# Optimization experiments

Measured on AMD Instinct MI355X. Metric: run time of the kernel, lower is better.

Reference implementation:

```python
import jax, jax.numpy as jnp
import numpy as np

N = 50000      # nodes
E = 600000     # edges (before self loops)
F_IN = 128     # num_features
HID = 64       # num_hidden (per-head out channels of conv1)
HEADS = 8
NCLS = 16      # num_classes
NC = 16        # n_components (k_ricci feature dim)
NCP = 16       # n_components_p (e_poinc feature dim)


def _glorot(key, shape):
    lim = float(np.sqrt(6.0 / (shape[0] + shape[1])))
    return jax.random.uniform(key, shape, jnp.float32, -lim, lim)


def setup_inputs() -> dict:
    key = jax.random.key(0)
    ks = jax.random.split(key, 16)
    H1 = HEADS * HID  # 512
    return {
        "x": jax.random.normal(ks[0], (N, F_IN), jnp.float32),
        "edge_index": jax.random.randint(ks[1], (2, E), 0, N, jnp.int32),
        "alpha": jnp.ones((), jnp.float32),  # alpha_hp scalar
        "k_ricci": jax.random.normal(ks[2], (E + N, NC), jnp.float32),
        "e_poinc": jax.random.normal(ks[3], (N, NCP), jnp.float32),
        # conv1 params
        "W_src1": _glorot(ks[4], (F_IN, H1)),
        "h1_w1": _glorot(ks[5], (NC, HID)),
        "h1_w2": _glorot(ks[6], (HID, HID)),
        "h1_b2": jnp.zeros((HID,), jnp.float32),
        "p1_w1": _glorot(ks[7], (NCP, H1)),
        "p1_w2": _glorot(ks[8], (H1, H1)),
        "p1_b2": jnp.zeros((H1,), jnp.float32),
        "bias1": jnp.zeros((H1,), jnp.float32),
        # conv2 params (heads=1, concat=False)
        "W_src2": _glorot(ks[9], (H1, NCLS)),
        "h2_w1": _glorot(ks[10], (NC, NCLS)),
        "h2_w2": _glorot(ks[11], (NCLS, NCLS)),
        "h2_b2": jnp.zeros((NCLS,), jnp.float32),
        "p2_w1": _glorot(ks[12], (NCP, NCLS)),
        "p2_w2": _glorot(ks[13], (NCLS, NCLS)),
        "p2_b2": jnp.zeros((NCLS,), jnp.float32),
        "bias2": jnp.zeros((NCLS,), jnp.float32),
    }


def _segment_softmax(logits, seg, n):
    # PyG-style softmax over variable-sized segments, per channel.
    m = jax.ops.segment_max(logits, seg, num_segments=n)
    e = jnp.exp(logits - m[seg])
    s = jax.ops.segment_sum(e, seg, num_segments=n)
    return e / (s[seg] + 1e-16)


def _gat_layer(x, src, dst, k_ricci, e_poinc, alpha_hp,
               W_src, hw1, hw2, hb2, pw1, pw2, pb2, bias, H, C, concat):
    n = x.shape[0]
    xh = (x @ W_src).reshape(n, H, C)                                   # [N,H,C]
    # hmpnn MLP on per-edge Ricci features, then segment-softmax over SOURCE node
    edge_w = jax.nn.leaky_relu(k_ricci @ hw1, 0.2) @ hw2 + hb2          # [E',C]
    a = _segment_softmax(edge_w, src, n)                                # [E',C]
    msg = a[:, None, :] * xh[src]                                       # [E',H,C]
    agg = jax.ops.segment_sum(msg, dst, num_segments=n)                 # [N,H,C]
    out = agg.reshape(n, H * C) if concat else agg.mean(axis=1)
    out = out + bias
    # ham MLP on per-node Poincare features (+ extra leaky_relu, slope 0.01)
    p = jax.nn.leaky_relu(jax.nn.leaky_relu(e_poinc @ pw1, 0.2) @ pw2 + pb2, 0.01)
    return out + alpha_hp * p


def reference(x, edge_index, alpha, k_ricci, e_poinc,
              W_src1, h1_w1, h1_w2, h1_b2, p1_w1, p1_w2, p1_b2, bias1,
              W_src2, h2_w1, h2_w2, h2_b2, p2_w1, p2_w2, p2_b2, bias2):
    n = x.shape[0]
    loops = jnp.arange(n, dtype=edge_index.dtype)
    src = jnp.concatenate([edge_index[0], loops])   # add_self_loops
    dst = jnp.concatenate([edge_index[1], loops])
    h = _gat_layer(x, src, dst, k_ricci, e_poinc, alpha,
                   W_src1, h1_w1, h1_w2, h1_b2, p1_w1, p1_w2, p1_b2, bias1,
                   HEADS, HID, True)
    h = jax.nn.relu(h)
    o = _gat_layer(h, src, dst, k_ricci, e_poinc, alpha,
                   W_src2, h2_w1, h2_w2, h2_b2, p2_w1, p2_w2, p2_b2, bias2,
                   1, NCLS, False)
    return jax.nn.log_softmax(o, axis=1)
```

## Files before the change

kernel.cpp:

```cpp
#include <hip/hip_runtime.h>
#include <math.h>

#define N_NODES 50000
#define M_PAD   50048
#define N_EDGES 600000
#define E_TOT   650000
#define F_IN    128
#define HID     64
#define HEADS   8
#define H1      512
#define NCLS    16
#define NC      16
#define NCP     16
#define NBLK    ((N_NODES + 255) / 256)
#define FRNG    (N_NODES / 8)
#define FBPR    128
#define FPER    ((E_TOT + FBPR - 1) / FBPR)

typedef unsigned short u16;
typedef unsigned char  u8;
typedef __attribute__((ext_vector_type(8))) short short8;
typedef __attribute__((ext_vector_type(4))) float f32x4;
typedef __attribute__((ext_vector_type(2))) float f32x2;

__device__ __forceinline__ float bf2f(u16 h) {
    return __uint_as_float(((unsigned)h) << 16);
}
__device__ __forceinline__ u16 f2bf(float f) {
    unsigned u = __float_as_uint(f);
    u += 0x7fffu + ((u >> 16) & 1u);
    return (u16)(u >> 16);
}
__device__ __forceinline__ int edge_src(const int* __restrict__ ei, int e) {
    return (e < N_EDGES) ? ei[e] : (e - N_EDGES);
}
__device__ __forceinline__ int edge_dst(const int* __restrict__ ei, int e) {
    return (e < N_EDGES) ? ei[N_EDGES + e] : (e - N_EDGES);
}

__device__ __forceinline__ void gload16(const void* g, void* l) {
    __builtin_amdgcn_global_load_lds(
        (const __attribute__((address_space(1))) unsigned int*)g,
        (__attribute__((address_space(3))) unsigned int*)l, 16, 0, 0);
}

__global__ __launch_bounds__(256) void count_k(const int* __restrict__ ei,
                                               int* __restrict__ src_cnt, int* __restrict__ dst_cnt) {
    int e = blockIdx.x * 256 + threadIdx.x;
    if (e >= E_TOT) return;
    atomicAdd(&src_cnt[edge_src(ei, e)], 1);
    atomicAdd(&dst_cnt[edge_dst(ei, e)], 1);
}

__global__ __launch_bounds__(256) void scanA_k(const int* __restrict__ src_cnt,
                                               const int* __restrict__ dst_cnt,
                                               int* __restrict__ partials) {
    int pass = blockIdx.x >= NBLK;
    int b = blockIdx.x - pass * NBLK;
    const int* cnt = pass ? dst_cnt : src_cnt;
    int idx = b * 256 + threadIdx.x;
    int v = (idx < N_NODES) ? cnt[idx] : 0;
    __shared__ int red[4];
    #pragma unroll
    for (int off = 32; off; off >>= 1) v += __shfl_down(v, off, 64);
    if ((threadIdx.x & 63) == 0) red[threadIdx.x >> 6] = v;
    __syncthreads();
    if (threadIdx.x == 0) partials[blockIdx.x] = red[0] + red[1] + red[2] + red[3];
}

__global__ __launch_bounds__(512) void scanB_k(int* __restrict__ partials) {
    __shared__ int lds[512];
    int t = threadIdx.x;
    int seg = t >> 8, i = t & 255;
    int v = (i < NBLK) ? partials[seg * NBLK + i] : 0;
    lds[t] = v;
    __syncthreads();
    for (int d = 1; d < 256; d <<= 1) {
        int x = (i >= d) ? lds[seg * 256 + i - d] : 0;
        __syncthreads();
        lds[t] += x;
        __syncthreads();
    }
    if (i < NBLK) partials[seg * NBLK + i] = lds[t] - v;
}

__global__ __launch_bounds__(256) void scanC_k(const int* __restrict__ src_cnt,
                                               const int* __restrict__ dst_cnt,
                                               const int* __restrict__ partials,
                                               int* __restrict__ src_off, int* __restrict__ dst_off) {
    int pass = blockIdx.x >= NBLK;
    int b = blockIdx.x - pass * NBLK;
    const int* cnt = pass ? dst_cnt : src_cnt;
    int* off = pass ? dst_off : src_off;
    int base = partials[blockIdx.x];
    __shared__ int lds[256];
    int t = threadIdx.x;
    int idx = b * 256 + t;
    int v = (idx < N_NODES) ? cnt[idx] : 0;
    lds[t] = v;
    __syncthreads();
    for (int d = 1; d < 256; d <<= 1) {
        int x = (t >= d) ? lds[t - d] : 0;
        __syncthreads();
        lds[t] += x;
        __syncthreads();
    }
    if (idx < N_NODES) off[idx] = base + lds[t] - v;
    if (b == 0 && t == 0) off[N_NODES] = E_TOT;
}

__global__ __launch_bounds__(256) void fillD_k(const int* __restrict__ ei,
                                               const int* __restrict__ dst_off, int* __restrict__ dst_cur,
                                               int* __restrict__ deid, int* __restrict__ dsrc) {
    const int range = blockIdx.x & 7, slice = blockIdx.x >> 3;
    const int d0 = range * FRNG, d1 = d0 + FRNG;
    const int e0 = slice * FPER;
    const int e1 = (e0 + FPER < E_TOT) ? e0 + FPER : E_TOT;
    for (int e = e0 + threadIdx.x; e < e1; e += 256) {
        int d = edge_dst(ei, e);
        if (d < d0 || d >= d1) continue;
        int rd = dst_off[d] + atomicAdd(&dst_cur[d], 1);
        deid[rd] = e;
        dsrc[rd] = edge_src(ei, e);
    }
}

__global__ __launch_bounds__(256) void fillS_k(const int* __restrict__ dsrc,
                                               const int* __restrict__ src_off, int* __restrict__ src_cur,
                                               int* __restrict__ src_list) {
    const int range = blockIdx.x & 7, slice = blockIdx.x >> 3;
    const int s0 = range * FRNG, s1 = s0 + FRNG;
    const int r0 = slice * FPER;
    const int r1 = (r0 + FPER < E_TOT) ? r0 + FPER : E_TOT;
    for (int rd = r0 + threadIdx.x; rd < r1; rd += 256) {
        int s = dsrc[rd];
        if (s < s0 || s >= s1) continue;
        src_list[src_off[s] + atomicAdd(&src_cur[s], 1)] = rd;
    }
}

__global__ __launch_bounds__(256) void conv_a_k(const float* __restrict__ A, u16* __restrict__ Ap,
                                                int M, int Mp, int K) {
    int i = blockIdx.x * 256 + threadIdx.x;
    int total = (K >> 3) * Mp;
    if (i >= total) return;
    int r = i % Mp;
    int kb = i / Mp;
    u16* o = Ap + (size_t)i * 8;
    u16 tmp[8];
    if (r < M) {
        const float* a = A + (size_t)r * K + kb * 8;
        #pragma unroll
        for (int j = 0; j < 8; ++j) tmp[j] = f2bf(a[j]);
    } else {
        #pragma unroll
        for (int j = 0; j < 8; ++j) tmp[j] = 0;
    }
    *(ushort4*)o = *(ushort4*)tmp;
    *(ushort4*)(o + 4) = *(ushort4*)(tmp + 4);
}

__global__ __launch_bounds__(256) void conv_b_k(const float* __restrict__ B, u16* __restrict__ Bp,
                                                int K, int N) {
    int i = blockIdx.x * 256 + threadIdx.x;
    int total = (K >> 3) * N;
    if (i >= total) return;
    int n = i % N;
    int kb = i / N;
    u16 tmp[8];
    #pragma unroll
    for (int j = 0; j < 8; ++j) tmp[j] = f2bf(B[(size_t)(kb * 8 + j) * N + n]);
    u16* o = Bp + (size_t)i * 8;
    *(ushort4*)o = *(ushort4*)tmp;
    *(ushort4*)(o + 4) = *(ushort4*)(tmp + 4);
}

__device__ __forceinline__ void wfrag_one(const float* W, u16* o, int i, int K, int N) {
    int j = i & 7, lane = (i >> 3) & 63, rest = i >> 9;
    int nt = rest % (N / 16), ks = rest / (N / 16);
    int lm = lane & 15, quad = lane >> 4;
    int k = ks * 32 + quad * 8 + j, n = nt * 16 + lm;
    o[i] = (k < K) ? f2bf(W[(size_t)k * N + n]) : (u16)0;
}
__global__ __launch_bounds__(256) void wfrag_all_k(
    const float* __restrict__ h1w1, const float* __restrict__ h1w2,
    const float* __restrict__ h2w1, const float* __restrict__ h2w2,
    u16* __restrict__ w1f, u16* __restrict__ w2f,
    u16* __restrict__ w3f, u16* __restrict__ w4f) {
    int i = blockIdx.x * 256 + threadIdx.x;
    if (i < 2048)      wfrag_one(h1w1, w1f, i, 16, 64);
    else if (i < 6144) wfrag_one(h1w2, w2f, i - 2048, 64, 64);
    else if (i < 6656) wfrag_one(h2w1, w3f, i - 6144, 16, 16);
    else if (i < 7168) wfrag_one(h2w2, w4f, i - 6656, 16, 16);
}

template<int EPI>
__global__ __launch_bounds__(256) void mfma_gemm_k(
    const u16* __restrict__ Ap, const u16* __restrict__ Bp, u16* __restrict__ C,
    int M, int Mp, int Nn, int K,
    const float* __restrict__ bias, const u16* __restrict__ extra,
    const float* __restrict__ bias2, const float* __restrict__ alpha_p)
{
    __shared__ __align__(16) u16 LB[4][4096];
    const int t = threadIdx.x;
    const int wave = t >> 6, lane = t & 63;
    const int wm = (wave >> 1) * 64, wn = (wave & 1) * 64;
    const int lm = lane & 15, quad = lane >> 4;

    const int nwg = (int)(gridDim.y << 2);
    const int bid = (int)(blockIdx.y * 4 + blockIdx.x);
    const int qq = nwg >> 3, rr8 = nwg & 7;
    const int xcd = bid & 7, idx = bid >> 3;
    const int wg = (xcd < rr8 ? xcd * (qq + 1) : rr8 * (qq + 1) + (xcd - rr8) * qq) + idx;
    const int bn = (wg & 3) * 128;
    const int bm = (wg >> 2) * 128;

    const char* Ab = (const char*)Ap;
    const char* Bb = (const char*)Bp;

    f32x4 acc[4][4] = {};
    const int NT = K >> 5;

    auto stage = [&](int buf, int ts) {
        const int kb0 = ts * 4;
        #pragma unroll
        for (int h = 0; h < 2; ++h) {
            const int ob = h * 4096 + wave * 1024;
            const int kb = kb0 + (ob >> 11);
            const int rem = (ob & 1024) + lane * 16;
            gload16(Ab + ((size_t)kb * Mp + bm) * 16 + rem, (char*)LB[buf] + ob);
            gload16(Bb + ((size_t)kb * Nn + bn) * 16 + rem, (char*)LB[2 + buf] + ob);
        }
    };
    auto compute = [&](int cb) {
        const u16* As = LB[cb];
        const u16* Bs = LB[2 + cb];
        short8 af[4], bfv[4];
        #pragma unroll
        for (int mi = 0; mi < 4; ++mi)
            af[mi] = *(const short8*)(As + quad * 1024 + (wm + mi * 16 + lm) * 8);
        #pragma unroll
        for (int nj = 0; nj < 4; ++nj)
            bfv[nj] = *(const short8*)(Bs + quad * 1024 + (wn + nj * 16 + lm) * 8);
        #pragma unroll
        for (int mi = 0; mi < 4; ++mi)
            #pragma unroll
            for (int nj = 0; nj < 4; ++nj)
                acc[mi][nj] = __builtin_amdgcn_mfma_f32_16x16x32_bf16(af[mi], bfv[nj], acc[mi][nj], 0, 0, 0);
    };

    stage(0, 0);
    __syncthreads();
    int cur = 0;
    for (int ts = 0; ts < NT - 1; ++ts) {
        stage(cur ^ 1, ts + 1);
        compute(cur);
        __syncthreads();
        cur ^= 1;
    }
    compute(cur);
    __syncthreads();

    float* Tf = (float*)LB;
    const int lrow = t & 63, chunk = t >> 6;
    const int col0 = chunk * 32;
    const float alpha = (EPI == 0) ? 0.f : *alpha_p;
    #pragma unroll
    for (int pass = 0; pass < 2; ++pass) {
        if ((wave >> 1) == pass) {
            #pragma unroll
            for (int mi = 0; mi < 4; ++mi)
                #pragma unroll
                for (int r4 = 0; r4 < 4; ++r4) {
                    const int lr = mi * 16 + quad * 4 + r4;
                    const int sw = (lr & 7) << 2;
                    #pragma unroll
                    for (int nj = 0; nj < 4; ++nj)
                        Tf[lr * 128 + ((wn + nj * 16 + lm) ^ sw)] = acc[mi][nj][r4];
                }
        }
        __syncthreads();
        const int rr = bm + pass * 64 + lrow;
        if (rr < M) {
            const int sw = (lrow & 7) << 2;
            float v[32];
            #pragma unroll
            for (int j4 = 0; j4 < 8; ++j4) {
                float4 f = *(const float4*)&Tf[lrow * 128 + ((col0 + j4 * 4) ^ sw)];
                v[j4 * 4] = f.x; v[j4 * 4 + 1] = f.y; v[j4 * 4 + 2] = f.z; v[j4 * 4 + 3] = f.w;
            }
            const int gc0 = bn + col0;
            u16 pk[32];
            if (EPI == 0) {
                #pragma unroll
                for (int j = 0; j < 32; ++j) pk[j] = f2bf(v[j]);
            } else {
                const u16* ex = extra + (size_t)rr * Nn + gc0;
                #pragma unroll
                for (int g = 0; g < 4; ++g) {
                    short8 e8 = *(const short8*)(ex + g * 8);
                    #pragma unroll
                    for (int j = 0; j < 8; ++j) {
                        const int cj = g * 8 + j;
                        float vv = v[cj] + bias[gc0 + cj];
                        vv = vv > 0.f ? vv : 0.01f * vv;
                        float o = bf2f((u16)e8[j]) + bias2[gc0 + cj] + alpha * vv;
                        o = fmaxf(o, 0.f);
                        pk[cj] = f2bf(o);
                    }
                }
            }
            #pragma unroll
            for (int g = 0; g < 4; ++g)
                *(short8*)(C + (size_t)rr * Nn + gc0 + g * 8) = *(const short8*)&pk[g * 8];
        }
        __syncthreads();
    }
}

__global__ __launch_bounds__(256) void gemm_t1_k(
    const float* __restrict__ ep, const float* __restrict__ W, u16* __restrict__ t1p)
{
    __shared__ float Bs[16][64];
    const int bm = blockIdx.y * 64, bn = blockIdx.x * 64;
    const int t = threadIdx.x;
    const int tx = t & 15, ty = t >> 4;
    *(float4*)&Bs[t >> 4][(t & 15) * 4] = *(const float4*)&W[(size_t)(t >> 4) * H1 + bn + (t & 15) * 4];
    __syncthreads();
    const int r0 = bm + ty * 4;
    const int c0 = bn + tx * 4;
    for (int i = 0; i < 4; ++i) {
        int r = r0 + i;
        if (r >= N_NODES) continue;
        float av[16];
        #pragma unroll
        for (int j4 = 0; j4 < 16; j4 += 4) {
            float4 v = *(const float4*)(ep + (size_t)r * NCP + j4);
            av[j4] = v.x; av[j4 + 1] = v.y; av[j4 + 2] = v.z; av[j4 + 3] = v.w;
        }
        u16 pk[4];
        #pragma unroll
        for (int q = 0; q < 4; ++q) {
            float s = 0.f;
            #pragma unroll
            for (int k = 0; k < 16; ++k) s = fmaf(av[k], Bs[k][tx * 4 + q], s);
            s = s > 0.f ? s : 0.2f * s;
            pk[q] = f2bf(s);
        }
        u16* o = t1p + ((size_t)(c0 >> 3) * M_PAD + r) * 8 + (c0 & 7);
        *(ushort4*)o = *(ushort4*)pk;
    }
}

__global__ __launch_bounds__(256) void gemm_n16_k(
    const u16* __restrict__ A, const float* __restrict__ B, float* __restrict__ C,
    int M, int K)
{
    __shared__ float As[16][64];
    __shared__ float Bs[64][16];
    const int row0 = blockIdx.x * 16;
    const int t = threadIdx.x;
    const int r = t >> 4, c = t & 15;
    const int ar = t >> 4, ak4 = (t & 15) * 4;
    const int bk = t >> 2, bc4 = (t & 3) * 4;
    float acc = 0.f;
    for (int k0 = 0; k0 < K; k0 += 64) {
        float4 av = make_float4(0.f, 0.f, 0.f, 0.f);
        if (row0 + ar < M) {
            ushort4 h4 = *(const ushort4*)(A + (size_t)(row0 + ar) * K + k0 + ak4);
            av = make_float4(bf2f(h4.x), bf2f(h4.y), bf2f(h4.z), bf2f(h4.w));
        }
        *(float4*)&As[ar][ak4] = av;
        *(float4*)&Bs[bk][bc4] = *(const float4*)(B + (size_t)(k0 + bk) * 16 + bc4);
        __syncthreads();
        #pragma unroll
        for (int kk = 0; kk < 64; ++kk)
            acc = fmaf(As[r][kk], Bs[kk][c], acc);
        __syncthreads();
    }
    if (row0 + r < M) C[(size_t)(row0 + r) * 16 + c] = acc;
}

#define TSTR 72
__global__ __launch_bounds__(256) void edge_mlps_k(
    const float* __restrict__ kr, const int* __restrict__ deid,
    const u16* __restrict__ w1f, const u16* __restrict__ w2f, const float* __restrict__ b2a,
    const u16* __restrict__ w3f, const u16* __restrict__ w4f, const float* __restrict__ b2b,
    u16* __restrict__ ebd, u16* __restrict__ ebd2)
{
    __shared__ __align__(16) u16 T[4][16 * TSTR];
    const int t = threadIdx.x, wv = t >> 6, lane = t & 63;
    const int lm = lane & 15, quad = lane >> 4;
    const int tile = blockIdx.x * 4 + wv;
    const int s0 = tile * 16;
    if (s0 >= E_TOT) return;
    u16* Tw = T[wv];

    short8 W1[4], W2[2][4];
    #pragma unroll
    for (int nt = 0; nt < 4; ++nt) W1[nt] = *(const short8*)(w1f + ((size_t)nt * 64 + lane) * 8);
    #pragma unroll
    for (int ks = 0; ks < 2; ++ks)
        #pragma unroll
        for (int nt = 0; nt < 4; ++nt)
            W2[ks][nt] = *(const short8*)(w2f + (((size_t)ks * 4 + nt) * 64 + lane) * 8);
    short8 W3 = *(const short8*)(w3f + (size_t)lane * 8);
    short8 W4 = *(const short8*)(w4f + (size_t)lane * 8);
    float b2av[4];
    #pragma unroll
    for (int nt = 0; nt < 4; ++nt) b2av[nt] = b2a[nt * 16 + lm];
    float b2bv = b2b[lm];

    const int e = deid[s0 + lm];
    short8 af = {};
    if (quad < 2) {
        const float* kp = kr + (size_t)e * NC + quad * 8;
        float4 v0 = *(const float4*)kp;
        float4 v1 = *(const float4*)(kp + 4);
        u16 tmp[8] = {f2bf(v0.x), f2bf(v0.y), f2bf(v0.z), f2bf(v0.w),
                      f2bf(v1.x), f2bf(v1.y), f2bf(v1.z), f2bf(v1.w)};
        af = *(const short8*)tmp;
    }

    f32x4 a1[4] = {};
    #pragma unroll
    for (int nt = 0; nt < 4; ++nt)
        a1[nt] = __builtin_amdgcn_mfma_f32_16x16x32_bf16(af, W1[nt], a1[nt], 0, 0, 0);
    #pragma unroll
    for (int nt = 0; nt < 4; ++nt)
        #pragma unroll
        for (int r = 0; r < 4; ++r) {
            float v = a1[nt][r];
            v = v > 0.f ? v : 0.2f * v;
            Tw[(quad * 4 + r) * TSTR + nt * 16 + lm] = f2bf(v);
        }
    __builtin_amdgcn_s_waitcnt(0);

    short8 a2[2];
    #pragma unroll
    for (int ks = 0; ks < 2; ++ks)
        a2[ks] = *(const short8*)&Tw[lm * TSTR + ks * 32 + quad * 8];
    f32x4 c2[4] = {};
    #pragma unroll
    for (int nt = 0; nt < 4; ++nt)
        #pragma unroll
        for (int ks = 0; ks < 2; ++ks)
            c2[nt] = __builtin_amdgcn_mfma_f32_16x16x32_bf16(a2[ks], W2[ks][nt], c2[nt], 0, 0, 0);
    #pragma unroll
    for (int nt = 0; nt < 4; ++nt)
        #pragma unroll
        for (int r = 0; r < 4; ++r)
            Tw[(quad * 4 + r) * TSTR + nt * 16 + lm] = f2bf(__expf(c2[nt][r] + b2av[nt]));
    __builtin_amdgcn_s_waitcnt(0);
    #pragma unroll
    for (int p = 0; p < 2; ++p) {
        int c = p * 64 + lane;
        int row = c >> 3, off = (c & 7) * 8;
        short8 v = *(const short8*)&Tw[row * TSTR + off];
        *(short8*)(ebd + (size_t)(s0 + row) * HID + off) = v;
    }

    f32x4 b1 = __builtin_amdgcn_mfma_f32_16x16x32_bf16(af, W3, (f32x4){}, 0, 0, 0);
    __builtin_amdgcn_s_waitcnt(0);
    #pragma unroll
    for (int r = 0; r < 4; ++r) {
        float v = b1[r];
        v = v > 0.f ? v : 0.2f * v;
        Tw[(quad * 4 + r) * TSTR + lm] = f2bf(v);
    }
    __builtin_amdgcn_s_waitcnt(0);
    short8 a3 = *(const short8*)&Tw[lm * TSTR + quad * 8];
    f32x4 c3 = __builtin_amdgcn_mfma_f32_16x16x32_bf16(a3, W4, (f32x4){}, 0, 0, 0);
    #pragma unroll
    for (int r = 0; r < 4; ++r)
        Tw[(quad * 4 + r) * TSTR + lm] = f2bf(__expf(c3[r] + b2bv));
    __builtin_amdgcn_s_waitcnt(0);
    if (lane < 32) {
        int row = lane >> 1, off = (lane & 1) * 8;
        short8 v = *(const short8*)&Tw[row * TSTR + off];
        *(short8*)(ebd2 + (size_t)(s0 + row) * NCLS + off) = v;
    }
}

__global__ __launch_bounds__(256) void s1inv_k(
    const u16* __restrict__ ebd, const int* __restrict__ src_off, const int* __restrict__ src_list,
    u16* __restrict__ xb)
{
    __shared__ float sinv[4][64];
    int gid = blockIdx.x * 256 + threadIdx.x;
    int wid = gid >> 6, lane = gid & 63, wv = threadIdx.x >> 6;
    if (wid >= N_NODES) return;
    int o0 = src_off[wid], o1 = src_off[wid + 1];
    float s0 = 0.f, s1 = 0.f, s2 = 0.f, s3 = 0.f;
    int i = o0;
    for (; i + 3 < o1; i += 4) {
        int l0 = src_list[i], l1 = src_list[i + 1], l2 = src_list[i + 2], l3 = src_list[i + 3];
        s0 += bf2f(ebd[(size_t)l0 * HID + lane]);
        s1 += bf2f(ebd[(size_t)l1 * HID + lane]);
        s2 += bf2f(ebd[(size_t)l2 * HID + lane]);
        s3 += bf2f(ebd[(size_t)l3 * HID + lane]);
    }
    for (; i < o1; ++i) {
        int sl = src_list[i];
        s0 += bf2f(ebd[(size_t)sl * HID + lane]);
    }
    sinv[wv][lane] = 1.f / (((s0 + s1) + (s2 + s3)) + 1e-16f);
    __builtin_amdgcn_s_waitcnt(0);

    const u16* xr = xb + (size_t)wid * H1 + lane * 8;
    short8 x8 = *(const short8*)xr;
    float y[8];
    #pragma unroll
    for (int j = 0; j < 8; ++j)
        y[j] = bf2f((u16)x8[j]) * sinv[wv][(lane * 8 + j) & 63];
    int p0 = 0, p1 = 0;
    p0 = __builtin_amdgcn_cvt_pk_fp8_f32(y[0], y[1], p0, false);
    p0 = __builtin_amdgcn_cvt_pk_fp8_f32(y[2], y[3], p0, true);
    p1 = __builtin_amdgcn_cvt_pk_fp8_f32(y[4], y[5], p1, false);
    p1 = __builtin_amdgcn_cvt_pk_fp8_f32(y[6], y[7], p1, true);
    uint2 pk; pk.x = (unsigned)p0; pk.y = (unsigned)p1;
    *(uint2*)((u8*)xb + (size_t)wid * (H1 * 2) + lane * 8) = pk;
}

__global__ __launch_bounds__(256) void msg1_k(
    const u16* __restrict__ ebd, const u8* __restrict__ xq,
    const int* __restrict__ dsrc, const int* __restrict__ dst_off,
    u16* __restrict__ aggb)
{
    int gid = blockIdx.x * 256 + threadIdx.x;
    int wid = gid >> 6, lane = gid & 63;
    if (wid >= N_NODES) return;
    int o0 = dst_off[wid], o1 = dst_off[wid + 1];
    const int a_off = (lane & 7) * 8;
    float acc[8] = {};
    int i = o0;
    for (; i + 3 < o1; i += 4) {
        int s0 = __builtin_nontemporal_load(dsrc + i);
        int s1 = __builtin_nontemporal_load(dsrc + i + 1);
        int s2 = __builtin_nontemporal_load(dsrc + i + 2);
        int s3 = __builtin_nontemporal_load(dsrc + i + 3);
        short8 a0 = __builtin_nontemporal_load((const short8*)(ebd + (size_t)i * HID + a_off));
        short8 a1 = __builtin_nontemporal_load((const short8*)(ebd + (size_t)(i + 1) * HID + a_off));
        short8 a2 = __builtin_nontemporal_load((const short8*)(ebd + (size_t)(i + 2) * HID + a_off));
        short8 a3 = __builtin_nontemporal_load((const short8*)(ebd + (size_t)(i + 3) * HID + a_off));
        uint2 q0 = *(const uint2*)(xq + (size_t)s0 * 1024 + lane * 8);
        uint2 q1 = *(const uint2*)(xq + (size_t)s1 * 1024 + lane * 8);
        uint2 q2 = *(const uint2*)(xq + (size_t)s2 * 1024 + lane * 8);
        uint2 q3 = *(const uint2*)(xq + (size_t)s3 * 1024 + lane * 8);
        const uint2 qs[4] = {q0, q1, q2, q3};
        const short8 as[4] = {a0, a1, a2, a3};
        #pragma unroll
        for (int u = 0; u < 4; ++u) {
            f32x2 d0 = __builtin_amdgcn_cvt_pk_f32_fp8((int)qs[u].x, false);
            f32x2 d1 = __builtin_amdgcn_cvt_pk_f32_fp8((int)qs[u].x, true);
            f32x2 d2 = __builtin_amdgcn_cvt_pk_f32_fp8((int)qs[u].y, false);
            f32x2 d3 = __builtin_amdgcn_cvt_pk_f32_fp8((int)qs[u].y, true);
            float xv[8] = {d0.x, d0.y, d1.x, d1.y, d2.x, d2.y, d3.x, d3.y};
            #pragma unroll
            for (int j = 0; j < 8; ++j)
                acc[j] = fmaf(bf2f((u16)as[u][j]), xv[j], acc[j]);
        }
    }
    for (; i < o1; ++i) {
        int s = __builtin_nontemporal_load(dsrc + i);
        short8 a8 = __builtin_nontemporal_load((const short8*)(ebd + (size_t)i * HID + a_off));
        uint2 q = *(const uint2*)(xq + (size_t)s * 1024 + lane * 8);
        f32x2 d0 = __builtin_amdgcn_cvt_pk_f32_fp8((int)q.x, false);
        f32x2 d1 = __builtin_amdgcn_cvt_pk_f32_fp8((int)q.x, true);
        f32x2 d2 = __builtin_amdgcn_cvt_pk_f32_fp8((int)q.y, false);
        f32x2 d3 = __builtin_amdgcn_cvt_pk_f32_fp8((int)q.y, true);
        float xv[8] = {d0.x, d0.y, d1.x, d1.y, d2.x, d2.y, d3.x, d3.y};
        #pragma unroll
        for (int j = 0; j < 8; ++j)
            acc[j] = fmaf(bf2f((u16)a8[j]), xv[j], acc[j]);
    }
    u16 pk[8];
    #pragma unroll
    for (int j = 0; j < 8; ++j) pk[j] = f2bf(acc[j]);
    __builtin_nontemporal_store(*(const short8*)pk, (short8*)(aggb + (size_t)wid * H1 + lane * 8));
}

__global__ __launch_bounds__(256) void s2sum_k(
    const u16* __restrict__ ebd2, const int* __restrict__ src_off, const int* __restrict__ src_list,
    float* __restrict__ inv2)
{
    int t = threadIdx.x;
    int g = blockIdx.x * 16 + (t >> 4), c = t & 15;
    if (g >= N_NODES) return;
    int o0 = src_off[g], o1 = src_off[g + 1];
    float sum = 0.f;
    for (int i = o0; i < o1; ++i) {
        int sl = src_list[i];
        sum += bf2f(ebd2[(size_t)sl * NCLS + c]);
    }
    inv2[(size_t)g * NCLS + c] = 1.f / (sum + 1e-16f);
}

__global__ __launch_bounds__(256) void msg2_k(
    const u16* __restrict__ ebd2, const float* __restrict__ inv2,
    const float* __restrict__ xh2, const int* __restrict__ dsrc,
    const int* __restrict__ dst_off, float* __restrict__ agg2)
{
    int t = threadIdx.x;
    int g = blockIdx.x * 16 + (t >> 4), c = t & 15;
    if (g >= N_NODES) return;
    int o0 = dst_off[g], o1 = dst_off[g + 1];
    float acc = 0.f;
    for (int i = o0; i < o1; ++i) {
        int s = dsrc[i];
        float a = bf2f(ebd2[(size_t)i * NCLS + c]) * inv2[(size_t)s * NCLS + c];
        acc = fmaf(a, xh2[(size_t)s * NCLS + c], acc);
    }
    agg2[(size_t)g * NCLS + c] = acc;
}

__global__ __launch_bounds__(256) void final_k(
    const float* __restrict__ agg2, const float* __restrict__ ep,
    const float* __restrict__ pw1, const float* __restrict__ pw2,
    const float* __restrict__ pb2, const float* __restrict__ bias,
    const float* __restrict__ alpha_p, float* __restrict__ out)
{
    __shared__ float s1w[256], s2w[256], sb[16], sbias[16];
    const int t = threadIdx.x;
    s1w[t] = pw1[t];
    s2w[t] = pw2[t];
    if (t < 16) { sb[t] = pb2[t]; sbias[t] = bias[t]; }
    __syncthreads();
    const int v = blockIdx.x * 256 + t;
    if (v >= N_NODES) return;
    float alpha = *alpha_p;
    float e_[16];
    #pragma unroll
    for (int j4 = 0; j4 < 16; j4 += 4) {
        float4 vv = *(const float4*)(ep + (size_t)v * 16 + j4);
        e_[j4] = vv.x; e_[j4 + 1] = vv.y; e_[j4 + 2] = vv.z; e_[j4 + 3] = vv.w;
    }
    float t2[16];
    #pragma unroll
    for (int c = 0; c < 16; ++c) {
        float s = 0.f;
        #pragma unroll
        for (int j = 0; j < 16; ++j) s = fmaf(e_[j], s1w[j * 16 + c], s);
        t2[c] = s > 0.f ? s : 0.2f * s;
    }
    float o[16];
    #pragma unroll
    for (int c4 = 0; c4 < 16; c4 += 4) {
        float4 ag = *(const float4*)(agg2 + (size_t)v * 16 + c4);
        float agv[4] = {ag.x, ag.y, ag.z, ag.w};
        #pragma unroll
        for (int q = 0; q < 4; ++q) {
            int c = c4 + q;
            float p = sb[c];
            #pragma unroll
            for (int j = 0; j < 16; ++j) p = fmaf(t2[j], s2w[j * 16 + c], p);
            p = p > 0.f ? p : 0.01f * p;
            o[c] = agv[q] + sbias[c] + alpha * p;
        }
    }
    float mx = o[0];
    #pragma unroll
    for (int c = 1; c < 16; ++c) mx = fmaxf(mx, o[c]);
    float se = 0.f;
    #pragma unroll
    for (int c = 0; c < 16; ++c) se += expf(o[c] - mx);
    float lse = mx + logf(se);
    #pragma unroll
    for (int c4 = 0; c4 < 16; c4 += 4)
        *(float4*)(out + (size_t)v * 16 + c4) =
            make_float4(o[c4] - lse, o[c4 + 1] - lse, o[c4 + 2] - lse, o[c4 + 3] - lse);
}

extern "C" void kernel_launch(void* const* d_in, const int* in_sizes, int n_in,
                              void* d_out, int out_size, void* d_ws, size_t ws_size,
                              hipStream_t stream) {
    const float* x    = (const float*)d_in[0];
    const int*   ei   = (const int*)d_in[1];
    const float* alpha= (const float*)d_in[2];
    const float* kr   = (const float*)d_in[3];
    const float* ep   = (const float*)d_in[4];
    const float* W1   = (const float*)d_in[5];
    const float* h1w1 = (const float*)d_in[6];
    const float* h1w2 = (const float*)d_in[7];
    const float* h1b2 = (const float*)d_in[8];
    const float* p1w1 = (const float*)d_in[9];
    const float* p1w2 = (const float*)d_in[10];
    const float* p1b2 = (const float*)d_in[11];
    const float* b1   = (const float*)d_in[12];
    const float* W2   = (const float*)d_in[13];
    const float* h2w1 = (const float*)d_in[14];
    const float* h2w2 = (const float*)d_in[15];
    const float* h2b2 = (const float*)d_in[16];
    const float* p2w1 = (const float*)d_in[17];
    const float* p2w2 = (const float*)d_in[18];
    const float* p2b2 = (const float*)d_in[19];
    const float* b2   = (const float*)d_in[20];
    float* out = (float*)d_out;

    char* p = (char*)d_ws;
    auto alloc = [&](size_t bytes) { char* r = p; p += (bytes + 255) & ~(size_t)255; return r; };

    char* r0    = alloc((size_t)64 * M_PAD * 16);
    u16*  xb    = (u16*)r0;
    u16*  t1p   = (u16*)r0;
    u16*  aggb  = (u16*)alloc((size_t)N_NODES * H1 * 2);
    char* ebr   = alloc((size_t)E_TOT * HID * 2);
    u16*  ebd   = (u16*)ebr;
    u16*  hb    = (u16*)ebr;
    u16*  ebd2  = (u16*)alloc((size_t)E_TOT * NCLS * 2);
    u16*  xp    = (u16*)alloc((size_t)16 * M_PAD * 16);
    u16*  W1p   = (u16*)alloc((size_t)16 * H1 * 16);
    u16*  p1w2p = (u16*)alloc((size_t)64 * H1 * 16);
    u16*  w1f   = (u16*)alloc(2048 * 2);
    u16*  w2f   = (u16*)alloc(4096 * 2);
    u16*  w3f   = (u16*)alloc(512 * 2);
    u16*  w4f   = (u16*)alloc(512 * 2);
    int* src_cnt  = (int*)alloc(N_NODES * 4);
    int* dst_cnt  = (int*)alloc(N_NODES * 4);
    int* src_cur  = (int*)alloc(N_NODES * 4);
    int* dst_cur  = (int*)alloc(N_NODES * 4);
    int* partials = (int*)alloc(2 * NBLK * 4);
    int* src_off  = (int*)alloc((N_NODES + 1) * 4);
    int* dst_off  = (int*)alloc((N_NODES + 1) * 4);
    int* src_list = (int*)alloc((size_t)E_TOT * 4);
    int* deid     = (int*)alloc((size_t)E_TOT * 4);
    int* dsrc     = (int*)alloc((size_t)E_TOT * 4);
    float* xh2  = (float*)alloc((size_t)N_NODES * NCLS * 4);
    float* agg2 = (float*)alloc((size_t)N_NODES * NCLS * 4);
    float* inv2 = (float*)alloc((size_t)N_NODES * NCLS * 4);

    const dim3 blk(256);
    const int EB = (E_TOT + 255) / 256;
    const int WB = (N_NODES * 64 + 255) / 256;
    const int GB16 = (N_NODES + 15) / 16;
    const dim3 gmm(512 / 128, M_PAD / 128);
    const int MLPB = (E_TOT / 16 + 3) / 4;

    hipMemsetAsync(src_cnt, 0, (char*)partials - (char*)src_cnt, stream);
    count_k<<<EB, blk, 0, stream>>>(ei, src_cnt, dst_cnt);
    scanA_k<<<2 * NBLK, blk, 0, stream>>>(src_cnt, dst_cnt, partials);
    scanB_k<<<1, 512, 0, stream>>>(partials);
    scanC_k<<<2 * NBLK, blk, 0, stream>>>(src_cnt, dst_cnt, partials, src_off, dst_off);
    fillD_k<<<8 * FBPR, blk, 0, stream>>>(ei, dst_off, dst_cur, deid, dsrc);
    fillS_k<<<8 * FBPR, blk, 0, stream>>>(dsrc, src_off, src_cur, src_list);
    conv_a_k<<<(16 * M_PAD + 255) / 256, blk, 0, stream>>>(x, xp, N_NODES, M_PAD, F_IN);
    conv_b_k<<<(16 * H1 + 255) / 256, blk, 0, stream>>>(W1, W1p, F_IN, H1);
    conv_b_k<<<(64 * H1 + 255) / 256, blk, 0, stream>>>(p1w2, p1w2p, H1, H1);
    wfrag_all_k<<<28, blk, 0, stream>>>(h1w1, h1w2, h2w1, h2w2, w1f, w2f, w3f, w4f);

    mfma_gemm_k<0><<<gmm, blk, 0, stream>>>(xp, W1p, xb, N_NODES, M_PAD, H1, F_IN,
                                            nullptr, nullptr, nullptr, nullptr);
    edge_mlps_k<<<MLPB, blk, 0, stream>>>(kr, deid, w1f, w2f, h1b2, w3f, w4f, h2b2, ebd, ebd2);
    s1inv_k<<<WB, blk, 0, stream>>>(ebd, src_off, src_list, xb);
    msg1_k<<<WB, blk, 0, stream>>>(ebd, (const u8*)xb, dsrc, dst_off, aggb);
    gemm_t1_k<<<dim3(8, (N_NODES + 63) / 64), blk, 0, stream>>>(ep, p1w1, t1p);
    mfma_gemm_k<3><<<gmm, blk, 0, stream>>>(t1p, p1w2p, hb, N_NODES, M_PAD, H1, H1,
                                            p1b2, aggb, b1, alpha);

    gemm_n16_k<<<(N_NODES + 15) / 16, blk, 0, stream>>>(hb, W2, xh2, N_NODES, H1);
    s2sum_k<<<GB16, blk, 0, stream>>>(ebd2, src_off, src_list, inv2);
    msg2_k<<<GB16, blk, 0, stream>>>(ebd2, inv2, xh2, dsrc, dst_off, agg2);
    final_k<<<(N_NODES + 255) / 256, blk, 0, stream>>>(agg2, ep, p2w1, p2w2, p2b2, b2, alpha, out);
}
```

Baseline: 670.3 us.

## Fuse conv2 input projection into conv1 GEMM epilogue with partial-sum reduction

The epilogue of the second conv1 GEMM now multiplies each bf16-rounded hidden row by the 512x16 W_src2 slice it holds in shared memory. It writes four per-column-tile fp32 partial 16-wide results, and a small reduction kernel sums them. This removes the write and re-read of the 50000x512 bf16 hidden tensor and the separate gemm_n16 kernel. In exchange, the epilogue takes extra FMAs, shuffles and 8 KB more LDS, and adds one small kernel launch.

Result: no change. 673.8 us (+0.5%).

```diff
diff --git a/kernel.cpp b/kernel.cpp
--- a/kernel.cpp
+++ b/kernel.cpp
@@ -199,9 +199,10 @@
     const u16* __restrict__ Ap, const u16* __restrict__ Bp, u16* __restrict__ C,
     int M, int Mp, int Nn, int K,
     const float* __restrict__ bias, const u16* __restrict__ extra,
-    const float* __restrict__ bias2, const float* __restrict__ alpha_p)
+    const float* __restrict__ bias2, const float* __restrict__ alpha_p,
+    const float* __restrict__ W2, float* __restrict__ xh2p)
 {
-    __shared__ __align__(16) u16 LB[4][4096];
+    __shared__ __align__(16) char LSD[32768 + (EPI ? 8192 : 0)];
     const int t = threadIdx.x;
     const int wave = t >> 6, lane = t & 63;
     const int wm = (wave >> 1) * 64, wn = (wave & 1) * 64;
@@ -228,13 +229,13 @@
             const int ob = h * 4096 + wave * 1024;
             const int kb = kb0 + (ob >> 11);
             const int rem = (ob & 1024) + lane * 16;
-            gload16(Ab + ((size_t)kb * Mp + bm) * 16 + rem, (char*)LB[buf] + ob);
-            gload16(Bb + ((size_t)kb * Nn + bn) * 16 + rem, (char*)LB[2 + buf] + ob);
+            gload16(Ab + ((size_t)kb * Mp + bm) * 16 + rem, LSD + buf * 8192 + ob);
+            gload16(Bb + ((size_t)kb * Nn + bn) * 16 + rem, LSD + 16384 + buf * 8192 + ob);
         }
     };
     auto compute = [&](int cb) {
-        const u16* As = LB[cb];
-        const u16* Bs = LB[2 + cb];
+        const u16* As = (const u16*)(LSD + cb * 8192);
+        const u16* Bs = (const u16*)(LSD + 16384 + cb * 8192);
         short8 af[4], bfv[4];
         #pragma unroll
         for (int mi = 0; mi < 4; ++mi)
@@ -250,6 +251,12 @@
     };
 
     stage(0, 0);
+    if (EPI != 0) {
+        const char* Wg = (const char*)(W2 + (size_t)bn * 16);
+        const int off = wave * 2048;
+        gload16(Wg + off + lane * 16, LSD + 32768 + off);
+        gload16(Wg + off + 1024 + lane * 16, LSD + 32768 + off + 1024);
+    }
     __syncthreads();
     int cur = 0;
     for (int ts = 0; ts < NT - 1; ++ts) {
@@ -261,9 +268,8 @@
     compute(cur);
     __syncthreads();
 
-    float* Tf = (float*)LB;
-    const int lrow = t & 63, chunk = t >> 6;
-    const int col0 = chunk * 32;
+    float* Tf = (float*)LSD;
+    const float* W2s = (const float*)(LSD + 32768);
     const float alpha = (EPI == 0) ? 0.f : *alpha_p;
     #pragma unroll
     for (int pass = 0; pass < 2; ++pass) {
@@ -280,21 +286,42 @@
                 }
         }
         __syncthreads();
-        const int rr = bm + pass * 64 + lrow;
-        if (rr < M) {
-            const int sw = (lrow & 7) << 2;
-            float v[32];
-            #pragma unroll
-            for (int j4 = 0; j4 < 8; ++j4) {
-                float4 f = *(const float4*)&Tf[lrow * 128 + ((col0 + j4 * 4) ^ sw)];
-                v[j4 * 4] = f.x; v[j4 * 4 + 1] = f.y; v[j4 * 4 + 2] = f.z; v[j4 * 4 + 3] = f.w;
-            }
-            const int gc0 = bn + col0;
-            u16 pk[32];
-            if (EPI == 0) {
+        if (EPI == 0) {
+            const int lrow = t & 63, chunk = t >> 6;
+            const int col0 = chunk * 32;
+            const int rr = bm + pass * 64 + lrow;
+            if (rr < M) {
+                const int sw = (lrow & 7) << 2;
+                float v[32];
+                #pragma unroll
+                for (int j4 = 0; j4 < 8; ++j4) {
+                    float4 f = *(const float4*)&Tf[lrow * 128 + ((col0 + j4 * 4) ^ sw)];
+                    v[j4 * 4] = f.x; v[j4 * 4 + 1] = f.y; v[j4 * 4 + 2] = f.z; v[j4 * 4 + 3] = f.w;
+                }
+                const int gc0 = bn + col0;
+                u16 pk[32];
                 #pragma unroll
                 for (int j = 0; j < 32; ++j) pk[j] = f2bf(v[j]);
-            } else {
+                #pragma unroll
+                for (int g = 0; g < 4; ++g)
+                    *(short8*)(C + (size_t)rr * Nn + gc0 + g * 8) = *(const short8*)&pk[g * 8];
+            }
+        } else {
+            const int row = wave * 16 + lm;
+            const int col0 = quad * 32;
+            const int rr = bm + pass * 64 + row;
+            const int gc0 = bn + col0;
+            float a16[16];
+            #pragma unroll
+            for (int c = 0; c < 16; ++c) a16[c] = 0.f;
+            if (rr < M) {
+                const int sw = (row & 7) << 2;
+                float v[32];
+                #pragma unroll
+                for (int j4 = 0; j4 < 8; ++j4) {
+                    float4 f = *(const float4*)&Tf[row * 128 + ((col0 + j4 * 4) ^ sw)];
+                    v[j4 * 4] = f.x; v[j4 * 4 + 1] = f.y; v[j4 * 4 + 2] = f.z; v[j4 * 4 + 3] = f.w;
+                }
                 const u16* ex = extra + (size_t)rr * Nn + gc0;
                 #pragma unroll
                 for (int g = 0; g < 4; ++g) {
@@ -306,16 +333,53 @@
                         vv = vv > 0.f ? vv : 0.01f * vv;
                         float o = bf2f((u16)e8[j]) + bias2[gc0 + cj] + alpha * vv;
                         o = fmaxf(o, 0.f);
-                        pk[cj] = f2bf(o);
+                        float hq = bf2f(f2bf(o));
+                        const float* wr = W2s + (col0 + cj) * 16;
+                        float4 w0 = *(const float4*)(wr);
+                        float4 w1 = *(const float4*)(wr + 4);
+                        float4 w2q = *(const float4*)(wr + 8);
+                        float4 w3 = *(const float4*)(wr + 12);
+                        a16[0]  = fmaf(hq, w0.x, a16[0]);  a16[1]  = fmaf(hq, w0.y, a16[1]);
+                        a16[2]  = fmaf(hq, w0.z, a16[2]);  a16[3]  = fmaf(hq, w0.w, a16[3]);
+                        a16[4]  = fmaf(hq, w1.x, a16[4]);  a16[5]  = fmaf(hq, w1.y, a16[5]);
+                        a16[6]  = fmaf(hq, w1.z, a16[6]);  a16[7]  = fmaf(hq, w1.w, a16[7]);
+                        a16[8]  = fmaf(hq, w2q.x, a16[8]); a16[9]  = fmaf(hq, w2q.y, a16[9]);
+                        a16[10] = fmaf(hq, w2q.z, a16[10]); a16[11] = fmaf(hq, w2q.w, a16[11]);
+                        a16[12] = fmaf(hq, w3.x, a16[12]); a16[13] = fmaf(hq, w3.y, a16[13]);
+                        a16[14] = fmaf(hq, w3.z, a16[14]); a16[15] = fmaf(hq, w3.w, a16[15]);
                     }
                 }
+                #pragma unroll
+                for (int c = 0; c < 16; ++c) {
+                    a16[c] += __shfl_xor(a16[c], 16, 64);
+                    a16[c] += __shfl_xor(a16[c], 32, 64);
+                }
+                if (quad == 0) {
+                    float* dst = xh2p + ((size_t)(bn >> 7) * M_PAD + rr) * 16;
+                    *(float4*)(dst + 0)  = make_float4(a16[0], a16[1], a16[2], a16[3]);
+                    *(float4*)(dst + 4)  = make_float4(a16[4], a16[5], a16[6], a16[7]);
+                    *(float4*)(dst + 8)  = make_float4(a16[8], a16[9], a16[10], a16[11]);
+                    *(float4*)(dst + 12) = make_float4(a16[12], a16[13], a16[14], a16[15]);
+                }
             }
-            #pragma unroll
-            for (int g = 0; g < 4; ++g)
-                *(short8*)(C + (size_t)rr * Nn + gc0 + g * 8) = *(const short8*)&pk[g * 8];
         }
         __syncthreads();
     }
+}
+
+__global__ __launch_bounds__(256) void red4_k(const float* __restrict__ xh2p,
+                                              float* __restrict__ xh2) {
+    int i = blockIdx.x * 256 + threadIdx.x;
+    if (i >= N_NODES * 4) return;
+    const float4* P = (const float4*)xh2p;
+    const size_t S = (size_t)M_PAD * 4;
+    float4 a = P[i], b = P[S + i], c = P[2 * S + i], d = P[3 * S + i];
+    float4 r;
+    r.x = (a.x + b.x) + (c.x + d.x);
+    r.y = (a.y + b.y) + (c.y + d.y);
+    r.z = (a.z + b.z) + (c.z + d.z);
+    r.w = (a.w + b.w) + (c.w + d.w);
+    ((float4*)xh2)[i] = r;
 }
 
 __global__ __launch_bounds__(256) void gemm_t1_k(
@@ -350,35 +414,6 @@
         u16* o = t1p + ((size_t)(c0 >> 3) * M_PAD + r) * 8 + (c0 & 7);
         *(ushort4*)o = *(ushort4*)pk;
     }
-}
-
-__global__ __launch_bounds__(256) void gemm_n16_k(
-    const u16* __restrict__ A, const float* __restrict__ B, float* __restrict__ C,
-    int M, int K)
-{
-    __shared__ float As[16][64];
-    __shared__ float Bs[64][16];
-    const int row0 = blockIdx.x * 16;
-    const int t = threadIdx.x;
-    const int r = t >> 4, c = t & 15;
-    const int ar = t >> 4, ak4 = (t & 15) * 4;
-    const int bk = t >> 2, bc4 = (t & 3) * 4;
-    float acc = 0.f;
-    for (int k0 = 0; k0 < K; k0 += 64) {
-        float4 av = make_float4(0.f, 0.f, 0.f, 0.f);
-        if (row0 + ar < M) {
-            ushort4 h4 = *(const ushort4*)(A + (size_t)(row0 + ar) * K + k0 + ak4);
-            av = make_float4(bf2f(h4.x), bf2f(h4.y), bf2f(h4.z), bf2f(h4.w));
-        }
-        *(float4*)&As[ar][ak4] = av;
-        *(float4*)&Bs[bk][bc4] = *(const float4*)(B + (size_t)(k0 + bk) * 16 + bc4);
-        __syncthreads();
-        #pragma unroll
-        for (int kk = 0; kk < 64; ++kk)
-            acc = fmaf(As[r][kk], Bs[kk][c], acc);
-        __syncthreads();
-    }
-    if (row0 + r < M) C[(size_t)(row0 + r) * 16 + c] = acc;
 }
 
 #define TSTR 72
@@ -706,9 +741,10 @@
     u16*  aggb  = (u16*)alloc((size_t)N_NODES * H1 * 2);
     char* ebr   = alloc((size_t)E_TOT * HID * 2);
     u16*  ebd   = (u16*)ebr;
-    u16*  hb    = (u16*)ebr;
     u16*  ebd2  = (u16*)alloc((size_t)E_TOT * NCLS * 2);
-    u16*  xp    = (u16*)alloc((size_t)16 * M_PAD * 16);
+    char* xpr   = alloc((size_t)16 * M_PAD * 16);
+    u16*  xp    = (u16*)xpr;
+    float* xh2p = (float*)xpr;
     u16*  W1p   = (u16*)alloc((size_t)16 * H1 * 16);
     u16*  p1w2p = (u16*)alloc((size_t)64 * H1 * 16);
     u16*  w1f   = (u16*)alloc(2048 * 2);
@@ -749,15 +785,15 @@
     wfrag_all_k<<<28, blk, 0, stream>>>(h1w1, h1w2, h2w1, h2w2, w1f, w2f, w3f, w4f);
 
     mfma_gemm_k<0><<<gmm, blk, 0, stream>>>(xp, W1p, xb, N_NODES, M_PAD, H1, F_IN,
-                                            nullptr, nullptr, nullptr, nullptr);
+                                            nullptr, nullptr, nullptr, nullptr, nullptr, nullptr);
     edge_mlps_k<<<MLPB, blk, 0, stream>>>(kr, deid, w1f, w2f, h1b2, w3f, w4f, h2b2, ebd, ebd2);
     s1inv_k<<<WB, blk, 0, stream>>>(ebd, src_off, src_list, xb);
     msg1_k<<<WB, blk, 0, stream>>>(ebd, (const u8*)xb, dsrc, dst_off, aggb);
     gemm_t1_k<<<dim3(8, (N_NODES + 63) / 64), blk, 0, stream>>>(ep, p1w1, t1p);
-    mfma_gemm_k<3><<<gmm, blk, 0, stream>>>(t1p, p1w2p, hb, N_NODES, M_PAD, H1, H1,
-                                            p1b2, aggb, b1, alpha);
-
-    gemm_n16_k<<<(N_NODES + 15) / 16, blk, 0, stream>>>(hb, W2, xh2, N_NODES, H1);
+    mfma_gemm_k<3><<<gmm, blk, 0, stream>>>(t1p, p1w2p, nullptr, N_NODES, M_PAD, H1, H1,
+                                            p1b2, aggb, b1, alpha, W2, xh2p);
+    red4_k<<<(N_NODES * 4 + 255) / 256, blk, 0, stream>>>(xh2p, xh2);
+
     s2sum_k<<<GB16, blk, 0, stream>>>(ebd2, src_off, src_list, inv2);
     msg2_k<<<GB16, blk, 0, stream>>>(ebd2, inv2, xh2, dsrc, dst_off, agg2);
     final_k<<<(N_NODES + 255) / 256, blk, 0, stream>>>(agg2, ep, p2w1, p2w2, p2b2, b2, alpha, out);
```
